# Performance work log

Measured on AMD Instinct MI355X. Metric: run time of the kernel, lower is better.

Reference implementation:

```python
import jax, jax.numpy as jnp
import numpy as np

N_NODES = 10000
N_EDGES = 320000
IN_CH = 128
HID = 64
HEADS = 8
OUT_CH = 2
NEG_SLOPE = 0.2  # PyG GATConv default
EPS = 1e-16      # PyG softmax denominator eps


def setup_inputs() -> dict:
    key = jax.random.key(0)
    ks = jax.random.split(key, 12)
    x = jax.random.normal(ks[0], (N_NODES, IN_CH), dtype=jnp.float32)
    edge_index = jax.random.randint(ks[1], (2, N_EDGES), 0, N_NODES, dtype=jnp.int64)
    s = 0.05
    W1 = jax.random.normal(ks[2], (IN_CH, HEADS * HID), dtype=jnp.float32) * s
    a_src1 = jax.random.normal(ks[3], (HEADS, HID), dtype=jnp.float32) * s
    a_dst1 = jax.random.normal(ks[4], (HEADS, HID), dtype=jnp.float32) * s
    b1 = jnp.zeros((HEADS * HID,), dtype=jnp.float32)
    W2 = jax.random.normal(ks[5], (HEADS * HID, HID), dtype=jnp.float32) * s
    a_src2 = jax.random.normal(ks[6], (1, HID), dtype=jnp.float32) * s
    a_dst2 = jax.random.normal(ks[7], (1, HID), dtype=jnp.float32) * s
    b2 = jnp.zeros((HID,), dtype=jnp.float32)
    Wc = jax.random.normal(ks[8], (HID, OUT_CH), dtype=jnp.float32) * s
    bc = jnp.zeros((OUT_CH,), dtype=jnp.float32)
    return dict(x=x, edge_index=edge_index, W1=W1, a_src1=a_src1, a_dst1=a_dst1,
                b1=b1, W2=W2, a_src2=a_src2, a_dst2=a_dst2, b2=b2, Wc=Wc, bc=bc)


def gat_layer(x, src, dst, W, a_src, a_dst, bias, heads, ch, concat):
    # x: [N, F_in]; src/dst: [E] (self-loops already appended)
    N = x.shape[0]
    h = (x @ W).reshape(N, heads, ch)                 # [N, H, C]
    e_src = jnp.einsum('nhc,hc->nh', h, a_src)        # [N, H]
    e_dst = jnp.einsum('nhc,hc->nh', h, a_dst)
    e = jax.nn.leaky_relu(e_src[src] + e_dst[dst], NEG_SLOPE)  # [E, H]
    # segment softmax over destination nodes (max-shift has zero gradient)
    m = jax.lax.stop_gradient(jax.ops.segment_max(e, dst, num_segments=N))
    w = jnp.exp(e - m[dst])
    denom = jax.ops.segment_sum(w, dst, num_segments=N)
    alpha = w / (denom[dst] + EPS)                    # [E, H]
    # scatter-aggregate weighted source features
    out = jax.ops.segment_sum(h[src] * alpha[:, :, None], dst, num_segments=N)  # [N,H,C]
    out = out.reshape(N, heads * ch) if concat else out.mean(axis=1)
    return out + bias


def reference(x, edge_index, W1, a_src1, a_dst1, b1, W2, a_src2, a_dst2, b2, Wc, bc):
    N = x.shape[0]
    loop = jnp.arange(N, dtype=edge_index.dtype)
    src = jnp.concatenate([edge_index[0], loop])  # PyG add_self_loops=True
    dst = jnp.concatenate([edge_index[1], loop])
    h1 = gat_layer(x, src, dst, W1, a_src1, a_dst1, b1, HEADS, HID, True)
    h1 = jax.nn.elu(h1)
    # dropout is identity in eval mode
    h2 = gat_layer(h1, src, dst, W2, a_src2, a_dst2, b2, 1, HID, False)
    return h2 @ Wc + bc  # [N, 2]
```

## Files before the change

kernel.cpp:

```cpp
#include <hip/hip_runtime.h>
#include <hip/hip_bf16.h>

#define N_NODES 10000
#define N_EDGES 320000
#define IN_CH 128
#define HID 64
#define HEADS 8
#define OUT_CH 2
#define BM 64
#define BK 16
#define BCAP 128
#define MPAD 10048

typedef __attribute__((ext_vector_type(8))) short frag8;
typedef __attribute__((ext_vector_type(4))) float f32x4;

__device__ __forceinline__ unsigned short f2bf(float f) {
    union { float f; unsigned u; } v; v.f = f;
    unsigned r = (v.u + 0x7FFFu + ((v.u >> 16) & 1u)) >> 16;
    return (unsigned short)r;
}

__device__ __forceinline__ void g2l16(const void* g, void* l) {
    __builtin_amdgcn_global_load_lds(
        (__attribute__((address_space(1))) unsigned int*)g,
        (__attribute__((address_space(3))) unsigned int*)l, 16, 0, 0);
}

__global__ __launch_bounds__(256) void prep_split(
    const float* __restrict__ x, const float* __restrict__ W1,
    unsigned short* __restrict__ xh, unsigned short* __restrict__ xl,
    unsigned short* __restrict__ w1h, unsigned short* __restrict__ w1l,
    int* __restrict__ cursor) {
    int bx = blockIdx.x, tid = threadIdx.x;
    if (bx < 628) {
        int idx = bx * 256 + tid;
        int row = idx >> 4, c = idx & 15;
        float f[8];
        if (row < N_NODES) {
            float4 v0 = *(const float4*)&x[(size_t)row * IN_CH + c * 8];
            float4 v1 = *(const float4*)&x[(size_t)row * IN_CH + c * 8 + 4];
            f[0] = v0.x; f[1] = v0.y; f[2] = v0.z; f[3] = v0.w;
            f[4] = v1.x; f[5] = v1.y; f[6] = v1.z; f[7] = v1.w;
        } else {
            #pragma unroll
            for (int j = 0; j < 8; j++) f[j] = 0.f;
        }
        unsigned short hb[8], lb[8];
        #pragma unroll
        for (int j = 0; j < 8; j++) {
            hb[j] = f2bf(f[j]);
            float hf = __uint_as_float((unsigned)hb[j] << 16);
            lb[j] = f2bf(f[j] - hf);
        }
        size_t o = ((size_t)row * 16 + (c ^ (row & 15))) * 8;
        *(ushort4*)&xh[o]     = make_ushort4(hb[0], hb[1], hb[2], hb[3]);
        *(ushort4*)&xh[o + 4] = make_ushort4(hb[4], hb[5], hb[6], hb[7]);
        *(ushort4*)&xl[o]     = make_ushort4(lb[0], lb[1], lb[2], lb[3]);
        *(ushort4*)&xl[o + 4] = make_ushort4(lb[4], lb[5], lb[6], lb[7]);
    } else if (bx < 660) {
        int idx = (bx - 628) * 256 + tid;
        int kb = idx >> 9, c = idx & 511;
        int hh = c >> 6, cc = c & 63;
        unsigned short hb[8], lb[8];
        #pragma unroll
        for (int i = 0; i < 8; i++) {
            float v = W1[(size_t)(kb * 8 + i) * (HEADS * HID) + c];
            hb[i] = f2bf(v);
            float hf = __uint_as_float((unsigned)hb[i] << 16);
            lb[i] = f2bf(v - hf);
        }
        size_t o = (((size_t)hh * 16 + kb) * 64 + cc) * 8;
        *(ushort4*)&w1h[o]     = make_ushort4(hb[0], hb[1], hb[2], hb[3]);
        *(ushort4*)&w1h[o + 4] = make_ushort4(hb[4], hb[5], hb[6], hb[7]);
        *(ushort4*)&w1l[o]     = make_ushort4(lb[0], lb[1], lb[2], lb[3]);
        *(ushort4*)&w1l[o + 4] = make_ushort4(lb[4], lb[5], lb[6], lb[7]);
    } else {
        int idx = (bx - 660) * 256 + tid;
        if (idx < 2500) *(int4*)&cursor[idx * 4] = make_int4(0, 0, 0, 0);
    }
}

__global__ __launch_bounds__(256) void gemm1_mfma(
    const unsigned short* __restrict__ xh, const unsigned short* __restrict__ xl,
    const unsigned short* __restrict__ w1h, const unsigned short* __restrict__ w1l,
    const float* __restrict__ a_src1, const float* __restrict__ a_dst1,
    unsigned short* __restrict__ hfeatP,
    float* __restrict__ esAll, float* __restrict__ edAll, int M) {
    __shared__ alignas(16) unsigned short Ah[8192];
    __shared__ alignas(16) unsigned short Al[8192];
    __shared__ alignas(16) unsigned short Bh[8192];
    __shared__ alignas(16) unsigned short Bl[8192];
    int tid = threadIdx.x;
    int lane = tid & 63, w = tid >> 6;
    int vb = (blockIdx.x & 7) * 157 + (blockIdx.x >> 3);
    int h  = vb & 7;
    int bm = (vb >> 3) * BM;

    {
        const unsigned short* gAh = xh  + (size_t)bm * 128;
        const unsigned short* gAl = xl  + (size_t)bm * 128;
        const unsigned short* gBh = w1h + (size_t)h * 8192;
        const unsigned short* gBl = w1l + (size_t)h * 8192;
        #pragma unroll
        for (int i = 0; i < 4; i++) {
            int s = w * 4 + i;
            int go = s * 512 + lane * 8;
            g2l16(gAh + go, &Ah[s * 512]);
            g2l16(gAl + go, &Al[s * 512]);
            g2l16(gBh + go, &Bh[s * 512]);
            g2l16(gBl + go, &Bl[s * 512]);
        }
    }
    __syncthreads();

    int col = lane & 15, g4 = lane >> 4;
    int arow = w * 16 + col;
    f32x4 acc[4] = {};
    #pragma unroll
    for (int ks = 0; ks < 4; ks++) {
        int ai = (arow * 16 + ((ks * 4 + g4) ^ col)) * 8;
        frag8 ah = *(const frag8*)&Ah[ai];
        frag8 al = *(const frag8*)&Al[ai];
        #pragma unroll
        for (int ct = 0; ct < 4; ct++) {
            int bi = ((ks * 4 + g4) * 64 + ct * 16 + col) * 8;
            frag8 bhv = *(const frag8*)&Bh[bi];
            frag8 blv = *(const frag8*)&Bl[bi];
            acc[ct] = __builtin_amdgcn_mfma_f32_16x16x32_bf16(ah, bhv, acc[ct], 0, 0, 0);
            acc[ct] = __builtin_amdgcn_mfma_f32_16x16x32_bf16(al, bhv, acc[ct], 0, 0, 0);
            acc[ct] = __builtin_amdgcn_mfma_f32_16x16x32_bf16(ah, blv, acc[ct], 0, 0, 0);
        }
    }

    float asv[4], adv[4];
    #pragma unroll
    for (int ct = 0; ct < 4; ct++) {
        asv[ct] = a_src1[h * 64 + ct * 16 + col];
        adv[ct] = a_dst1[h * 64 + ct * 16 + col];
    }
    #pragma unroll
    for (int r = 0; r < 4; r++) {
        float s = 0.f, d = 0.f;
        #pragma unroll
        for (int ct = 0; ct < 4; ct++) {
            s += acc[ct][r] * asv[ct];
            d += acc[ct][r] * adv[ct];
        }
        #pragma unroll
        for (int off = 1; off < 16; off <<= 1) {
            s += __shfl_xor(s, off, 64);
            d += __shfl_xor(d, off, 64);
        }
        if (col == 0) {
            int gr = bm + w * 16 + g4 * 4 + r;
            if (gr < M) {
                esAll[(size_t)h * M + gr] = s;
                edAll[(size_t)h * M + gr] = d;
            }
        }
    }

    __syncthreads();
    unsigned short* Tr = Ah;
    int wrow = w * 16 + g4 * 4;
    #pragma unroll
    for (int ct = 0; ct < 4; ct++)
        #pragma unroll
        for (int r = 0; r < 4; r++)
            Tr[(wrow + r) * 68 + ct * 16 + col] = f2bf(acc[ct][r]);
    __syncthreads();
    int row = tid >> 2, q = tid & 3;
    int gr = bm + row;
    if (gr < M) {
        int tb = row * 68 + q * 16;
        ushort4 t0 = *(const ushort4*)&Tr[tb];
        ushort4 t1 = *(const ushort4*)&Tr[tb + 4];
        ushort4 t2 = *(const ushort4*)&Tr[tb + 8];
        ushort4 t3 = *(const ushort4*)&Tr[tb + 12];
        unsigned short* dst =
            &hfeatP[(((size_t)(h >> 1) * M + gr) * 128) + (h & 1) * 64 + q * 16];
        *(ushort4*)&dst[0]  = t0;
        *(ushort4*)&dst[4]  = t1;
        *(ushort4*)&dst[8]  = t2;
        *(ushort4*)&dst[12] = t3;
    }
}

__global__ void fill_bucket(const int* __restrict__ src,
                            const int* __restrict__ dst, int E,
                            int* cursor, int* __restrict__ bucket) {
    int i = blockIdx.x * blockDim.x + threadIdx.x;
    if (i < E) {
        int d = dst[i];
        int pos = atomicAdd(&cursor[d], 1);
        bucket[(d << 7) + min(pos, BCAP - 1)] = src[i];
    }
}

__global__ __launch_bounds__(256) void gemm2_splitk(
    const float* __restrict__ h1,
    const float* __restrict__ W2,
    float* __restrict__ partial,
    int M) {
    __shared__ float As[BK][BM + 4];
    __shared__ float Bs[BK][64 + 4];
    int tid = threadIdx.x;
    int bm = blockIdx.x * BM;
    int h  = blockIdx.y;
    const float* B = W2 + (size_t)h * 64 * 64;
    float* C = partial + (size_t)h * M * 64;
    int tx = tid & 15, ty = tid >> 4;
    float acc[4][4] = {};
    for (int k0 = 0; k0 < 64; k0 += BK) {
        #pragma unroll
        for (int i = 0; i < 4; i++) {
            int e = tid + i * 256;
            int r = e >> 4, c = e & 15;
            int gr = bm + r;
            As[c][r] = (gr < M)
                ? h1[(size_t)gr * 512 + h * 64 + k0 + c] : 0.f;
        }
        #pragma unroll
        for (int i = 0; i < 4; i++) {
            int e = tid + i * 256;
            int r = e >> 6, c = e & 63;
            Bs[r][c] = B[(size_t)(k0 + r) * 64 + c];
        }
        __syncthreads();
        #pragma unroll
        for (int k = 0; k < BK; k++) {
            float4 a4 = *(const float4*)&As[k][ty * 4];
            float4 b4 = *(const float4*)&Bs[k][tx * 4];
            float a[4] = {a4.x, a4.y, a4.z, a4.w};
            float b[4] = {b4.x, b4.y, b4.z, b4.w};
            #pragma unroll
            for (int i = 0; i < 4; i++)
                #pragma unroll
                for (int j = 0; j < 4; j++) acc[i][j] += a[i] * b[j];
        }
        __syncthreads();
    }
    #pragma unroll
    for (int i = 0; i < 4; i++) {
        int gr = bm + ty * 4 + i;
        if (gr >= M) continue;
        #pragma unroll
        for (int j = 0; j < 4; j++)
            C[(size_t)gr * 64 + tx * 4 + j] = acc[i][j];
    }
}

__global__ __launch_bounds__(256) void gemm2_reduce(
    const float* __restrict__ partial,
    const float* __restrict__ a_src2, const float* __restrict__ a_dst2,
    float* __restrict__ hfeat2, float* __restrict__ es2, float* __restrict__ ed2,
    int M) {
    int n = blockIdx.x * 4 + (threadIdx.x >> 6);
    int l = threadIdx.x & 63;
    if (n >= M) return;
    float v = 0.f;
    #pragma unroll
    for (int h = 0; h < 8; h++)
        v += partial[(size_t)h * M * 64 + (size_t)n * 64 + l];
    hfeat2[(size_t)n * 64 + l] = v;
    float s = v * a_src2[l], t = v * a_dst2[l];
    #pragma unroll
    for (int off = 32; off; off >>= 1) {
        s += __shfl_down(s, off, 64);
        t += __shfl_down(t, off, 64);
    }
    if (l == 0) { es2[n] = s; ed2[n] = t; }
}

__global__ __launch_bounds__(256) void gat_agg_pair(
    const unsigned short* __restrict__ hfeatP, const float* __restrict__ esAll,
    const float* __restrict__ edAll, const int* __restrict__ bucket,
    const int* __restrict__ cursor, const float* __restrict__ b1,
    float* __restrict__ h1, int M) {
    int bx = blockIdx.x;
    int p = bx & 3;
    int n = (bx >> 2) * 4 + (threadIdx.x >> 6);
    int l = threadIdx.x & 63;
    int g = l >> 4;
    int q = l & 15;
    int hq = q >> 3;
    int sub = l & 31;
    int hs = l >> 5;
    int g4 = g << 2;
    int hbaseB = hq << 7;
    const char* hptr = (const char*)hfeatP + (size_t)p * M * 256 + (q << 4);
    const float* esS = esAll + (size_t)(p * 2 + hs) * M;
    float ednS = edAll[(size_t)(p * 2 + hs) * M + n];
    int start = n << 7;
    int deg = min(cursor[n], 96);
    int total = deg + 1;

    float a[8] = {};
    float dloc = 0.f;
    for (int base = 0; base < total; base += 32) {
        int idx = base + sub;
        int sld = bucket[start + idx];
        int sv = (idx < deg) ? sld : n;
        float wgt = 0.f;
        if (idx <= deg) {
            float e = esS[sv] + ednS;
            e = (e > 0.f) ? e : 0.2f * e;
            wgt = __expf(e);
        }
        dloc += wgt;
        int rb = sv << 8;
        int wb = __float_as_int(wgt);
        int cnt = min(32, total - base);
        for (int i = 0; i < cnt; i += 4) {
            int b0 = (i << 2) + g4;
            int rbg = __builtin_amdgcn_ds_bpermute(b0, rb);
            float wg = __int_as_float(
                __builtin_amdgcn_ds_bpermute(b0 + hbaseB, wb));
            const uint4 hv = *(const uint4*)(hptr + rbg);
            a[0] += wg * __uint_as_float(hv.x << 16);
            a[1] += wg * __uint_as_float(hv.x & 0xFFFF0000u);
            a[2] += wg * __uint_as_float(hv.y << 16);
            a[3] += wg * __uint_as_float(hv.y & 0xFFFF0000u);
            a[4] += wg * __uint_as_float(hv.z << 16);
            a[5] += wg * __uint_as_float(hv.z & 0xFFFF0000u);
            a[6] += wg * __uint_as_float(hv.w << 16);
            a[7] += wg * __uint_as_float(hv.w & 0xFFFF0000u);
        }
    }
    #pragma unroll
    for (int off = 16; off; off >>= 1) dloc += __shfl_xor(dloc, off, 64);
    float dother = __shfl_xor(dloc, 32, 64);
    #pragma unroll
    for (int k = 0; k < 8; k++) {
        a[k] += __shfl_xor(a[k], 16, 64);
        a[k] += __shfl_xor(a[k], 32, 64);
    }
    if (g == 0) {
        float d = (hq == 0) ? dloc : dother;
        d += 1e-16f;
        float inv = __builtin_amdgcn_rcpf(d);
        inv = inv * __fmaf_rn(-d, inv, 2.0f);
        const float4 b0v = *(const float4*)&b1[p * 128 + q * 8];
        const float4 b4v = *(const float4*)&b1[p * 128 + q * 8 + 4];
        float vv[8];
        vv[0] = a[0] * inv + b0v.x; vv[1] = a[1] * inv + b0v.y;
        vv[2] = a[2] * inv + b0v.z; vv[3] = a[3] * inv + b0v.w;
        vv[4] = a[4] * inv + b4v.x; vv[5] = a[5] * inv + b4v.y;
        vv[6] = a[6] * inv + b4v.z; vv[7] = a[7] * inv + b4v.w;
        #pragma unroll
        for (int k = 0; k < 8; k++)
            vv[k] = (vv[k] > 0.f) ? vv[k] : (__expf(vv[k]) - 1.f);
        float* dst = &h1[(size_t)n * 512 + p * 128 + q * 8];
        *(float4*)dst = make_float4(vv[0], vv[1], vv[2], vv[3]);
        *(float4*)(dst + 4) = make_float4(vv[4], vv[5], vv[6], vv[7]);
    }
}

__global__ __launch_bounds__(256) void gat_agg2(
    const float* __restrict__ hfeat2, const float* __restrict__ es,
    const float* __restrict__ ed, const int* __restrict__ bucket,
    const int* __restrict__ cursor, const float* __restrict__ b2,
    const float* __restrict__ Wc, const float* __restrict__ bc,
    float* __restrict__ out) {
    int n = blockIdx.x * 4 + (threadIdx.x >> 6);
    int l = threadIdx.x & 63;
    int g = l >> 4;
    int q = l & 15;
    int g4 = g << 2;
    int qoff = q << 4;
    int start = n << 7;
    int deg = min(cursor[n], 96);
    int total = deg + 1;
    float edn = ed[n];

    float ax = 0.f, ay = 0.f, az = 0.f, aw = 0.f;
    float dloc = 0.f;
    for (int base = 0; base < total; base += 64) {
        int cnt = min(64, total - base);
        float wgt = 0.f;
        int sv = n;
        if (l < cnt) {
            int idx = base + l;
            sv = (idx < deg) ? bucket[start + idx] : n;
            float e = es[sv] + edn;
            e = (e > 0.f) ? e : 0.2f * e;
            wgt = __expf(e);
        }
        dloc += wgt;
        int rb = sv << 8;
        int wb = __float_as_int(wgt);
        for (int i = 0; i < cnt; i += 4) {
            int bidx = (i << 2) + g4;
            int rbg = __builtin_amdgcn_ds_bpermute(bidx, rb);
            float wg = __int_as_float(__builtin_amdgcn_ds_bpermute(bidx, wb));
            const float4 hv = *(const float4*)((const char*)hfeat2 + (rbg + qoff));
            ax += wg * hv.x;
            ay += wg * hv.y;
            az += wg * hv.z;
            aw += wg * hv.w;
        }
    }
    float d = dloc;
    #pragma unroll
    for (int off = 32; off; off >>= 1) d += __shfl_down(d, off, 64);
    d = __shfl(d, 0, 64) + 1e-16f;
    float inv = __builtin_amdgcn_rcpf(d);
    inv = inv * __fmaf_rn(-d, inv, 2.0f);
    ax += __shfl_down(ax, 32, 64); ay += __shfl_down(ay, 32, 64);
    az += __shfl_down(az, 32, 64); aw += __shfl_down(aw, 32, 64);
    ax += __shfl_down(ax, 16, 64); ay += __shfl_down(ay, 16, 64);
    az += __shfl_down(az, 16, 64); aw += __shfl_down(aw, 16, 64);
    float p0 = 0.f, p1 = 0.f;
    if (g == 0) {
        const float4 bq = *(const float4*)&b2[q * 4];
        float h0 = ax * inv + bq.x, h1v = ay * inv + bq.y;
        float h2v = az * inv + bq.z, h3 = aw * inv + bq.w;
        const float2* WcV = (const float2*)Wc;
        float2 w0 = WcV[q * 4 + 0], w1 = WcV[q * 4 + 1];
        float2 w2 = WcV[q * 4 + 2], w3 = WcV[q * 4 + 3];
        p0 = h0 * w0.x + h1v * w1.x + h2v * w2.x + h3 * w3.x;
        p1 = h0 * w0.y + h1v * w1.y + h2v * w2.y + h3 * w3.y;
    }
    #pragma unroll
    for (int off = 1; off < 16; off <<= 1) {
        p0 += __shfl_xor(p0, off, 64);
        p1 += __shfl_xor(p1, off, 64);
    }
    if (l == 0) {
        out[n * 2 + 0] = p0 + bc[0];
        out[n * 2 + 1] = p1 + bc[1];
    }
}

extern "C" void kernel_launch(void* const* d_in, const int* in_sizes, int n_in,
                              void* d_out, int out_size, void* d_ws, size_t ws_size,
                              hipStream_t stream) {
    const float* x      = (const float*)d_in[0];
    const int*   eidx   = (const int*)d_in[1];
    const float* W1     = (const float*)d_in[2];
    const float* a_src1 = (const float*)d_in[3];
    const float* a_dst1 = (const float*)d_in[4];
    const float* b1     = (const float*)d_in[5];
    const float* W2     = (const float*)d_in[6];
    const float* a_src2 = (const float*)d_in[7];
    const float* a_dst2 = (const float*)d_in[8];
    const float* b2     = (const float*)d_in[9];
    const float* Wc     = (const float*)d_in[10];
    const float* bc     = (const float*)d_in[11];
    float* out = (float*)d_out;

    const int N = N_NODES, E = N_EDGES;
    const int* esrc = eidx;
    const int* edst = eidx + E;

    size_t off = 0;
    auto alloc = [&](size_t bytes) {
        void* p = (char*)d_ws + off;
        off += (bytes + 255) & ~(size_t)255;
        return p;
    };
    int*   cursor   = (int*)alloc((size_t)N * 4);
    int*   bucket   = (int*)alloc((size_t)N * BCAP * 4);
    unsigned short* hfeatP = (unsigned short*)alloc((size_t)4 * N * 128 * 2);
    float* h1       = (float*)alloc((size_t)N * 512 * 4);
    float* partial  = (float*)alloc((size_t)HEADS * N * 64 * 4);
    float* hfeat2   = (float*)alloc((size_t)N * 64 * 4);
    float* esAll    = (float*)alloc((size_t)HEADS * N * 4);
    float* edAll    = (float*)alloc((size_t)HEADS * N * 4);
    float* es2      = (float*)alloc((size_t)N * 4);
    float* ed2      = (float*)alloc((size_t)N * 4);
    unsigned short* xh  = (unsigned short*)alloc((size_t)MPAD * 128 * 2);
    unsigned short* xl  = (unsigned short*)alloc((size_t)MPAD * 128 * 2);
    unsigned short* w1h = (unsigned short*)alloc((size_t)128 * 512 * 2);
    unsigned short* w1l = (unsigned short*)alloc((size_t)128 * 512 * 2);

    prep_split<<<670, 256, 0, stream>>>(x, W1, xh, xl, w1h, w1l, cursor);
    gemm1_mfma<<<157 * 8, 256, 0, stream>>>(xh, xl, w1h, w1l, a_src1, a_dst1,
                                            hfeatP, esAll, edAll, N);
    fill_bucket<<<(E + 255) / 256, 256, 0, stream>>>(esrc, edst, E, cursor, bucket);
    gat_agg_pair<<<(N / 4) * 4, 256, 0, stream>>>(hfeatP, esAll, edAll,
                                                  bucket, cursor, b1, h1, N);
    dim3 gg2((N + BM - 1) / BM, HEADS);
    gemm2_splitk<<<gg2, 256, 0, stream>>>(h1, W2, partial, N);
    gemm2_reduce<<<(N + 3) / 4, 256, 0, stream>>>(partial, a_src2, a_dst2,
                                                  hfeat2, es2, ed2, N);
    gat_agg2<<<(N + 3) / 4, 256, 0, stream>>>(hfeat2, es2, ed2, bucket, cursor,
                                              b2, Wc, bc, out);
}
```

Baseline: 183.2 us.

## Replace FP32 split-K GEMM2 and reduce with bf16x3 MFMA GEMM and fused attention dots

```diff
diff --git a/kernel.cpp b/kernel.cpp
--- a/kernel.cpp
+++ b/kernel.cpp
@@ -29,8 +29,10 @@
 
 __global__ __launch_bounds__(256) void prep_split(
     const float* __restrict__ x, const float* __restrict__ W1,
+    const float* __restrict__ W2,
     unsigned short* __restrict__ xh, unsigned short* __restrict__ xl,
     unsigned short* __restrict__ w1h, unsigned short* __restrict__ w1l,
+    unsigned short* __restrict__ w2h, unsigned short* __restrict__ w2l,
     int* __restrict__ cursor) {
     int bx = blockIdx.x, tid = threadIdx.x;
     if (bx < 628) {
@@ -75,8 +77,24 @@
         *(ushort4*)&w1h[o + 4] = make_ushort4(hb[4], hb[5], hb[6], hb[7]);
         *(ushort4*)&w1l[o]     = make_ushort4(lb[0], lb[1], lb[2], lb[3]);
         *(ushort4*)&w1l[o + 4] = make_ushort4(lb[4], lb[5], lb[6], lb[7]);
+    } else if (bx < 676) {
+        int idx = (bx - 660) * 256 + tid;
+        int kb = idx >> 6, c = idx & 63;
+        unsigned short hb[8], lb[8];
+        #pragma unroll
+        for (int i = 0; i < 8; i++) {
+            float v = W2[(size_t)(kb * 8 + i) * 64 + c];
+            hb[i] = f2bf(v);
+            float hf = __uint_as_float((unsigned)hb[i] << 16);
+            lb[i] = f2bf(v - hf);
+        }
+        size_t o = ((size_t)kb * 64 + c) * 8;
+        *(ushort4*)&w2h[o]     = make_ushort4(hb[0], hb[1], hb[2], hb[3]);
+        *(ushort4*)&w2h[o + 4] = make_ushort4(hb[4], hb[5], hb[6], hb[7]);
+        *(ushort4*)&w2l[o]     = make_ushort4(lb[0], lb[1], lb[2], lb[3]);
+        *(ushort4*)&w2l[o + 4] = make_ushort4(lb[4], lb[5], lb[6], lb[7]);
     } else {
-        int idx = (bx - 660) * 256 + tid;
+        int idx = (bx - 676) * 256 + tid;
         if (idx < 2500) *(int4*)&cursor[idx * 4] = make_int4(0, 0, 0, 0);
     }
 }
@@ -198,89 +216,94 @@
     }
 }
 
-__global__ __launch_bounds__(256) void gemm2_splitk(
-    const float* __restrict__ h1,
-    const float* __restrict__ W2,
-    float* __restrict__ partial,
-    int M) {
-    __shared__ float As[BK][BM + 4];
-    __shared__ float Bs[BK][64 + 4];
-    int tid = threadIdx.x;
-    int bm = blockIdx.x * BM;
-    int h  = blockIdx.y;
-    const float* B = W2 + (size_t)h * 64 * 64;
-    float* C = partial + (size_t)h * M * 64;
-    int tx = tid & 15, ty = tid >> 4;
-    float acc[4][4] = {};
-    for (int k0 = 0; k0 < 64; k0 += BK) {
-        #pragma unroll
-        for (int i = 0; i < 4; i++) {
-            int e = tid + i * 256;
-            int r = e >> 4, c = e & 15;
-            int gr = bm + r;
-            As[c][r] = (gr < M)
-                ? h1[(size_t)gr * 512 + h * 64 + k0 + c] : 0.f;
-        }
-        #pragma unroll
-        for (int i = 0; i < 4; i++) {
-            int e = tid + i * 256;
-            int r = e >> 6, c = e & 63;
-            Bs[r][c] = B[(size_t)(k0 + r) * 64 + c];
-        }
-        __syncthreads();
-        #pragma unroll
-        for (int k = 0; k < BK; k++) {
-            float4 a4 = *(const float4*)&As[k][ty * 4];
-            float4 b4 = *(const float4*)&Bs[k][tx * 4];
-            float a[4] = {a4.x, a4.y, a4.z, a4.w};
-            float b[4] = {b4.x, b4.y, b4.z, b4.w};
-            #pragma unroll
-            for (int i = 0; i < 4; i++)
-                #pragma unroll
-                for (int j = 0; j < 4; j++) acc[i][j] += a[i] * b[j];
-        }
-        __syncthreads();
-    }
-    #pragma unroll
-    for (int i = 0; i < 4; i++) {
-        int gr = bm + ty * 4 + i;
-        if (gr >= M) continue;
-        #pragma unroll
-        for (int j = 0; j < 4; j++)
-            C[(size_t)gr * 64 + tx * 4 + j] = acc[i][j];
-    }
-}
-
-__global__ __launch_bounds__(256) void gemm2_reduce(
-    const float* __restrict__ partial,
+__global__ __launch_bounds__(256) void gemm2_mfma(
+    const unsigned short* __restrict__ h1h, const unsigned short* __restrict__ h1l,
+    const unsigned short* __restrict__ w2h, const unsigned short* __restrict__ w2l,
     const float* __restrict__ a_src2, const float* __restrict__ a_dst2,
     float* __restrict__ hfeat2, float* __restrict__ es2, float* __restrict__ ed2,
     int M) {
-    int n = blockIdx.x * 4 + (threadIdx.x >> 6);
-    int l = threadIdx.x & 63;
-    if (n >= M) return;
-    float v = 0.f;
-    #pragma unroll
-    for (int h = 0; h < 8; h++)
-        v += partial[(size_t)h * M * 64 + (size_t)n * 64 + l];
-    hfeat2[(size_t)n * 64 + l] = v;
-    float s = v * a_src2[l], t = v * a_dst2[l];
-    #pragma unroll
-    for (int off = 32; off; off >>= 1) {
-        s += __shfl_down(s, off, 64);
-        t += __shfl_down(t, off, 64);
-    }
-    if (l == 0) { es2[n] = s; ed2[n] = t; }
+    __shared__ alignas(16) unsigned short Ah[8192];
+    __shared__ alignas(16) unsigned short Al[8192];
+    __shared__ alignas(16) unsigned short Bh[8192];
+    __shared__ alignas(16) unsigned short Bl[8192];
+    int tid = threadIdx.x;
+    int lane = tid & 63, w = tid >> 6;
+    int bm = blockIdx.x * 64;
+    int col = lane & 15, g4 = lane >> 4;
+    int arow = w * 16 + col;
+
+    f32x4 acc[4] = {};
+    for (int t = 0; t < 4; t++) {
+        #pragma unroll
+        for (int i = 0; i < 4; i++) {
+            int s = w * 4 + i;
+            int lrow = s * 4 + (lane >> 4);
+            int cc = lane & 15;
+            int gc = t * 16 + (cc ^ (lrow & 15));
+            size_t goA = ((size_t)(bm + lrow) * 64 + gc) * 8;
+            g2l16(h1h + goA, &Ah[s * 512]);
+            g2l16(h1l + goA, &Al[s * 512]);
+            size_t goB = ((size_t)t * 1024 + s * 64 + lane) * 8;
+            g2l16(w2h + goB, &Bh[s * 512]);
+            g2l16(w2l + goB, &Bl[s * 512]);
+        }
+        __syncthreads();
+        #pragma unroll
+        for (int ks = 0; ks < 4; ks++) {
+            int ai = (arow * 16 + ((ks * 4 + g4) ^ col)) * 8;
+            frag8 ah = *(const frag8*)&Ah[ai];
+            frag8 al = *(const frag8*)&Al[ai];
+            #pragma unroll
+            for (int ct = 0; ct < 4; ct++) {
+                int bi = ((ks * 4 + g4) * 64 + ct * 16 + col) * 8;
+                frag8 bhv = *(const frag8*)&Bh[bi];
+                frag8 blv = *(const frag8*)&Bl[bi];
+                acc[ct] = __builtin_amdgcn_mfma_f32_16x16x32_bf16(ah, bhv, acc[ct], 0, 0, 0);
+                acc[ct] = __builtin_amdgcn_mfma_f32_16x16x32_bf16(al, bhv, acc[ct], 0, 0, 0);
+                acc[ct] = __builtin_amdgcn_mfma_f32_16x16x32_bf16(ah, blv, acc[ct], 0, 0, 0);
+            }
+        }
+        __syncthreads();
+    }
+
+    float asv[4], adv[4];
+    #pragma unroll
+    for (int ct = 0; ct < 4; ct++) {
+        asv[ct] = a_src2[ct * 16 + col];
+        adv[ct] = a_dst2[ct * 16 + col];
+    }
+    #pragma unroll
+    for (int r = 0; r < 4; r++) {
+        int gr = bm + w * 16 + g4 * 4 + r;
+        float s = 0.f, d = 0.f;
+        #pragma unroll
+        for (int ct = 0; ct < 4; ct++) {
+            s += acc[ct][r] * asv[ct];
+            d += acc[ct][r] * adv[ct];
+        }
+        #pragma unroll
+        for (int off = 1; off < 16; off <<= 1) {
+            s += __shfl_xor(s, off, 64);
+            d += __shfl_xor(d, off, 64);
+        }
+        if (gr < M) {
+            #pragma unroll
+            for (int ct = 0; ct < 4; ct++)
+                hfeat2[(size_t)gr * 64 + ct * 16 + col] = acc[ct][r];
+            if (col == 0) { es2[gr] = s; ed2[gr] = d; }
+        }
+    }
 }
 
 __global__ __launch_bounds__(256) void gat_agg_pair(
     const unsigned short* __restrict__ hfeatP, const float* __restrict__ esAll,
     const float* __restrict__ edAll, const int* __restrict__ bucket,
     const int* __restrict__ cursor, const float* __restrict__ b1,
-    float* __restrict__ h1, int M) {
+    unsigned short* __restrict__ h1h, unsigned short* __restrict__ h1l, int M) {
     int bx = blockIdx.x;
-    int p = bx & 3;
-    int n = (bx >> 2) * 4 + (threadIdx.x >> 6);
+    int p = (bx & 7) >> 1;
+    int nb = ((bx >> 3) << 1) + (bx & 1);
+    int n = nb * 4 + (threadIdx.x >> 6);
     int l = threadIdx.x & 63;
     int g = l >> 4;
     int q = l & 15;
@@ -351,9 +374,18 @@
         #pragma unroll
         for (int k = 0; k < 8; k++)
             vv[k] = (vv[k] > 0.f) ? vv[k] : (__expf(vv[k]) - 1.f);
-        float* dst = &h1[(size_t)n * 512 + p * 128 + q * 8];
-        *(float4*)dst = make_float4(vv[0], vv[1], vv[2], vv[3]);
-        *(float4*)(dst + 4) = make_float4(vv[4], vv[5], vv[6], vv[7]);
+        unsigned short hh[8], hl[8];
+        #pragma unroll
+        for (int k = 0; k < 8; k++) {
+            hh[k] = f2bf(vv[k]);
+            float hf = __uint_as_float((unsigned)hh[k] << 16);
+            hl[k] = f2bf(vv[k] - hf);
+        }
+        size_t o = ((size_t)n * 64 + p * 16 + q) * 8;
+        *(ushort4*)&h1h[o]     = make_ushort4(hh[0], hh[1], hh[2], hh[3]);
+        *(ushort4*)&h1h[o + 4] = make_ushort4(hh[4], hh[5], hh[6], hh[7]);
+        *(ushort4*)&h1l[o]     = make_ushort4(hl[0], hl[1], hl[2], hl[3]);
+        *(ushort4*)&h1l[o + 4] = make_ushort4(hl[4], hl[5], hl[6], hl[7]);
     }
 }
 
@@ -463,8 +495,8 @@
     int*   cursor   = (int*)alloc((size_t)N * 4);
     int*   bucket   = (int*)alloc((size_t)N * BCAP * 4);
     unsigned short* hfeatP = (unsigned short*)alloc((size_t)4 * N * 128 * 2);
-    float* h1       = (float*)alloc((size_t)N * 512 * 4);
-    float* partial  = (float*)alloc((size_t)HEADS * N * 64 * 4);
+    unsigned short* h1h = (unsigned short*)alloc((size_t)MPAD * 512 * 2);
+    unsigned short* h1l = (unsigned short*)alloc((size_t)MPAD * 512 * 2);
     float* hfeat2   = (float*)alloc((size_t)N * 64 * 4);
     float* esAll    = (float*)alloc((size_t)HEADS * N * 4);
     float* edAll    = (float*)alloc((size_t)HEADS * N * 4);
@@ -474,17 +506,18 @@
     unsigned short* xl  = (unsigned short*)alloc((size_t)MPAD * 128 * 2);
     unsigned short* w1h = (unsigned short*)alloc((size_t)128 * 512 * 2);
     unsigned short* w1l = (unsigned short*)alloc((size_t)128 * 512 * 2);
-
-    prep_split<<<670, 256, 0, stream>>>(x, W1, xh, xl, w1h, w1l, cursor);
+    unsigned short* w2h = (unsigned short*)alloc((size_t)512 * 64 * 2);
+    unsigned short* w2l = (unsigned short*)alloc((size_t)512 * 64 * 2);
+
+    prep_split<<<686, 256, 0, stream>>>(x, W1, W2, xh, xl, w1h, w1l, w2h, w2l,
+                                        cursor);
     gemm1_mfma<<<157 * 8, 256, 0, stream>>>(xh, xl, w1h, w1l, a_src1, a_dst1,
                                             hfeatP, esAll, edAll, N);
     fill_bucket<<<(E + 255) / 256, 256, 0, stream>>>(esrc, edst, E, cursor, bucket);
     gat_agg_pair<<<(N / 4) * 4, 256, 0, stream>>>(hfeatP, esAll, edAll,
-                                                  bucket, cursor, b1, h1, N);
-    dim3 gg2((N + BM - 1) / BM, HEADS);
-    gemm2_splitk<<<gg2, 256, 0, stream>>>(h1, W2, partial, N);
-    gemm2_reduce<<<(N + 3) / 4, 256, 0, stream>>>(partial, a_src2, a_dst2,
-                                                  hfeat2, es2, ed2, N);
+                                                  bucket, cursor, b1, h1h, h1l, N);
+    gemm2_mfma<<<157, 256, 0, stream>>>(h1h, h1l, w2h, w2l, a_src2, a_dst2,
+                                        hfeat2, es2, ed2, N);
     gat_agg2<<<(N + 3) / 4, 256, 0, stream>>>(hfeat2, es2, ed2, bucket, cursor,
                                               b2, Wc, bc, out);
 }
```

Measured after the change: 172.5 us. -5.8%, faster.
